# Kernel tuning notes

Measured on AMD Instinct MI355X. Metric: run time of the kernel, lower is better.

The kernel has to match this reference:

```python
import jax, jax.numpy as jnp
import numpy as np

N = 16384      # nodes
E = 524288     # edges (avg degree 32)
F_IN = 128     # input features
H1 = 256       # first_gcn_dimensions
H2 = 256       # second_gcn_dimensions
D1 = 64        # first_dense_neurons
D2 = 2         # second_dense_neurons (fixed by EYE=ones(2))


def setup_inputs() -> dict:
    key = jax.random.key(0)
    ks = jax.random.split(key, 8)
    w = lambda k, shp: (jax.random.normal(k, shp, jnp.float32) * 0.05)
    return dict(
        features=jax.random.normal(ks[0], (N, F_IN), jnp.float32),
        edges=jax.random.randint(ks[1], (2, E), 0, N),
        W1=w(ks[2], (F_IN, H1)), b1=jnp.zeros((H1,), jnp.float32),
        W2=w(ks[3], (H1, H2)), b2=jnp.zeros((H2,), jnp.float32),
        fc1_w=w(ks[4], (D1, H2)), fc1_b=jnp.zeros((D1,), jnp.float32),
        fc2_w=w(ks[5], (D2, D1)), fc2_b=jnp.zeros((D2,), jnp.float32),
    )


def gcn_conv(x, W, b, src, dst, n):
    """PyG GCNConv: xW, add self-loops, symmetric D^-1/2 (A+I) D^-1/2 aggregation."""
    x = x @ W
    loops = jnp.arange(n)
    s = jnp.concatenate([src, loops])
    d = jnp.concatenate([dst, loops])
    deg = jax.ops.segment_sum(jnp.ones(s.shape, x.dtype), d, num_segments=n)
    dinv = jnp.where(deg > 0, jax.lax.rsqrt(deg), 0.0)
    msg = x[s] * (dinv[s] * dinv[d])[:, None]          # gather + scale
    return jax.ops.segment_sum(msg, d, num_segments=n) + b  # scatter-add


def reference(features, edges, W1, b1, W2, b2, fc1_w, fc1_b, fc2_w, fc2_b):
    n = features.shape[0]
    src, dst = edges[0], edges[1]
    h1 = jax.nn.relu(gcn_conv(features, W1, b1, src, dst, n))
    h2 = gcn_conv(h1, W2, b2, src, dst, n)                 # [N, H2]
    a1 = jnp.tanh(h2 @ fc1_w.T + fc1_b)                    # [N, D1]
    assignment = jax.nn.softmax(a1 @ fc2_w.T + fc2_b, axis=1)  # [N, 2]
    group_features = assignment.T @ h2                     # [2, H2]
    # to_dense_adj: dense NxN adjacency, duplicate edges accumulate
    adj = jnp.zeros((n, n), h2.dtype).at[src, dst].add(1.0)
    new_adj = assignment.T @ (adj @ assignment)            # [2, 2]
    positive = jnp.clip(group_features[0][None, :], -100.0, 100.0)
    negative = jnp.clip(group_features[1][None, :], -100.0, 100.0)
    # F.normalize(p=1, dim=1) with eps=1e-12
    denom = jnp.maximum(jnp.sum(jnp.abs(new_adj), axis=1, keepdims=True), 1e-12)
    norm_diag = jnp.diag(new_adj / denom)
    pos_penalty = jnp.mean((norm_diag - 1.0) ** 2)         # MSE vs ones(2)
    graph_embedding = jnp.mean(group_features, axis=0, keepdims=True)  # [1, H2]
    return (graph_embedding, positive, negative, pos_penalty)
```

## Files before the change

### kernel.cpp

```cpp
#include <hip/hip_runtime.h>
#include <hip/hip_bf16.h>
#include <math.h>

#define N_NODES 16384
#define N_EDGES 524288
#define F_IN 128
#define H1 256
#define H2 256
#define D1 64
#define NA_GRID 512
#define DEG_CAP 96
#define SENT 16384

typedef __attribute__((ext_vector_type(8))) short short8;
typedef __attribute__((ext_vector_type(4))) float floatx4;
typedef unsigned short ushort_t;
typedef unsigned int uint_t;

__device__ inline float bf2f(ushort_t u) {
    union { uint_t i; float f; } v;
    v.i = ((uint_t)u) << 16;
    return v.f;
}
__device__ inline float u2f_lo(uint_t u) {
    union { uint_t i; float f; } v;
    v.i = u << 16;
    return v.f;
}
__device__ inline float u2f_hi(uint_t u) {
    union { uint_t i; float f; } v;
    v.i = u & 0xffff0000u;
    return v.f;
}
__device__ inline ushort_t f2bs(float x) {
    __hip_bfloat16 h = __float2bfloat16(x);
    return *reinterpret_cast<ushort_t*>(&h);
}
__device__ inline uint_t pack2(float lo, float hi) {
    return (uint_t)f2bs(lo) | ((uint_t)f2bs(hi) << 16);
}

__global__ __launch_bounds__(256) void prep_fill(
    const int* __restrict__ src, const int* __restrict__ dst,
    const float* __restrict__ W1, const float* __restrict__ W2,
    const float* __restrict__ fc1_w,
    int* __restrict__ cur, ushort_t* __restrict__ col,
    ushort_t* __restrict__ W1t, ushort_t* __restrict__ W2t,
    ushort_t* __restrict__ fc1bf) {
    int b = blockIdx.x, t = threadIdx.x;
    if (b < 2048) {
        int e = b * 256 + t;
        int d = dst[e];
        int pos = atomicAdd(&cur[d], 1);
        if (pos < DEG_CAP) col[d * DEG_CAP + pos] = (ushort_t)src[e];
    } else if (b < 2176) {
        int idx = (b - 2048) * 256 + t;
        int n = idx >> 7, k = idx & 127;
        W1t[idx] = f2bs(W1[k * 256 + n]);
    } else if (b < 2432) {
        int idx = (b - 2176) * 256 + t;
        int n = idx >> 8, k = idx & 255;
        W2t[idx] = f2bs(W2[k * 256 + n]);
    } else {
        int idx = (b - 2432) * 256 + t;
        fc1bf[idx] = f2bs(fc1_w[idx]);
    }
}

__global__ __launch_bounds__(256) void scale_feat(
    const float* __restrict__ features, const int* __restrict__ cnt,
    ushort_t* __restrict__ zs, ushort_t* __restrict__ bufY,
    ushort_t* __restrict__ col) {
    int b = blockIdx.x, t = threadIdx.x;
    if (b == 2048) {
        uint4 z4 = {0u, 0u, 0u, 0u};
        if (t < 16)
            *(uint4*)&zs[(size_t)SENT * 128 + t * 8] = z4;
        else if (t >= 64 && t < 96)
            *(uint4*)&bufY[(size_t)SENT * 256 + (t - 64) * 8] = z4;
        return;
    }
    int gid = b * 256 + t;
    int node = gid >> 5;
    int hl = gid & 31;
    int deg = cnt[node];
    float d = rsqrtf((float)(deg + 1));
    float4 v = *(const float4*)&features[gid * 4];
    uint2 p;
    p.x = pack2(v.x * d, v.y * d);
    p.y = pack2(v.z * d, v.w * d);
    *(uint2*)&zs[gid * 4] = p;
    if (deg < DEG_CAP) {
        int pad = (16 - (deg & 15)) & 15;
        if (hl < pad) col[node * DEG_CAP + deg + hl] = (ushort_t)SENT;
    }
}

__global__ __launch_bounds__(512, 8) void fused_layer1(
    const ushort_t* __restrict__ zs, const int* __restrict__ cnt,
    const ushort_t* __restrict__ col, const float* __restrict__ b1,
    const ushort_t* __restrict__ W1t, const ushort_t* __restrict__ W2t,
    ushort_t* __restrict__ bufY) {
    __shared__ __align__(16) ushort_t Az[16 * 136];
    __shared__ __align__(16) ushort_t Ah[16 * 264];
    const int tid = threadIdx.x;
    const int lane = tid & 63;
    const int wave = tid >> 6;
    const int m = lane & 15;
    const int quad = lane >> 4;
    const int row0 = blockIdx.x * 16;
    const uint_t* colu = (const uint_t*)col;

    for (int ii = 0; ii < 2; ++ii) {
        const int nl = wave * 2 + ii;
        const int node = __builtin_amdgcn_readfirstlane(row0 + nl);
        const int foff = lane * 2;
        const int deg = cnt[node];
        const int nb = (min(deg, DEG_CAP) + 15) >> 4;
        uint_t self = *(const uint_t*)&zs[(size_t)node * 128 + foff];
        float a0 = u2f_lo(self), a1 = u2f_hi(self);
        const int cb = node * (DEG_CAP / 2);
        for (int tb = 0; tb < nb; ++tb) {
            uint_t w[8];
            #pragma unroll
            for (int k = 0; k < 8; ++k) w[k] = colu[cb + tb * 8 + k];
            uint_t g[16];
            #pragma unroll
            for (int k = 0; k < 8; ++k) {
                int j0 = w[k] & 0xffff, j1 = w[k] >> 16;
                g[2 * k]     = *(const uint_t*)&zs[(size_t)j0 * 128 + foff];
                g[2 * k + 1] = *(const uint_t*)&zs[(size_t)j1 * 128 + foff];
            }
            #pragma unroll
            for (int q = 0; q < 16; ++q) {
                a0 += u2f_lo(g[q]); a1 += u2f_hi(g[q]);
            }
        }
        float dn = rsqrtf((float)(deg + 1));
        *(uint_t*)&Az[nl * 136 + foff] = pack2(a0 * dn, a1 * dn);
    }
    __syncthreads();

    const int wcol0 = wave * 32;
    floatx4 acc[2];
    const floatx4 zero4 = {0.f, 0.f, 0.f, 0.f};
    acc[0] = zero4; acc[1] = zero4;
    #pragma unroll
    for (int k0 = 0; k0 < 128; k0 += 32) {
        short8 a = *(const short8*)&Az[m * 136 + k0 + quad * 8];
        #pragma unroll
        for (int j = 0; j < 2; ++j) {
            short8 bb = *(const short8*)
                &W1t[(size_t)(wcol0 + j * 16 + m) * 128 + k0 + quad * 8];
            acc[j] = __builtin_amdgcn_mfma_f32_16x16x32_bf16(a, bb, acc[j], 0, 0, 0);
        }
    }
    #pragma unroll
    for (int j = 0; j < 2; ++j) {
        int cg = wcol0 + j * 16 + m;
        float bv = b1[cg];
        #pragma unroll
        for (int r = 0; r < 4; ++r) {
            float v = fmaxf(acc[j][r] + bv, 0.0f);
            Ah[(quad * 4 + r) * 264 + cg] = f2bs(v);
        }
    }
    __syncthreads();

    acc[0] = zero4; acc[1] = zero4;
    #pragma unroll
    for (int k0 = 0; k0 < 256; k0 += 32) {
        short8 a = *(const short8*)&Ah[m * 264 + k0 + quad * 8];
        #pragma unroll
        for (int j = 0; j < 2; ++j) {
            short8 bb = *(const short8*)
                &W2t[(size_t)(wcol0 + j * 16 + m) * 256 + k0 + quad * 8];
            acc[j] = __builtin_amdgcn_mfma_f32_16x16x32_bf16(a, bb, acc[j], 0, 0, 0);
        }
    }
    float rs4[4];
    #pragma unroll
    for (int r = 0; r < 4; ++r)
        rs4[r] = rsqrtf((float)(cnt[row0 + quad * 4 + r] + 1));
    #pragma unroll
    for (int j = 0; j < 2; ++j) {
        int cg = wcol0 + j * 16 + m;
        #pragma unroll
        for (int r = 0; r < 4; ++r)
            bufY[(size_t)(row0 + quad * 4 + r) * 256 + cg] = f2bs(acc[j][r] * rs4[r]);
    }
}

__global__ __launch_bounds__(512, 8) void agg2(
    const ushort_t* __restrict__ bufY, const int* __restrict__ cnt,
    const ushort_t* __restrict__ col, const float* __restrict__ b2,
    ushort_t* __restrict__ h2buf, int c0) {
    const int tid = threadIdx.x;
    const int lane = tid & 63;
    const int wave = tid >> 6;
    const int node = __builtin_amdgcn_readfirstlane(blockIdx.x * 8 + wave);
    const int coff = c0 + lane * 2;
    const int deg = cnt[node];
    const int nb = (min(deg, DEG_CAP) + 15) >> 4;
    uint_t self = *(const uint_t*)&bufY[(size_t)node * 256 + coff];
    float a0 = u2f_lo(self), a1 = u2f_hi(self);
    const uint_t* colu = (const uint_t*)col;
    const int cb = node * (DEG_CAP / 2);
    for (int tb = 0; tb < nb; ++tb) {
        uint_t w[8];
        #pragma unroll
        for (int k = 0; k < 8; ++k) w[k] = colu[cb + tb * 8 + k];
        uint_t g[16];
        #pragma unroll
        for (int k = 0; k < 8; ++k) {
            int j0 = w[k] & 0xffff, j1 = w[k] >> 16;
            g[2 * k]     = *(const uint_t*)&bufY[(size_t)j0 * 256 + coff];
            g[2 * k + 1] = *(const uint_t*)&bufY[(size_t)j1 * 256 + coff];
        }
        #pragma unroll
        for (int q = 0; q < 16; ++q) {
            a0 += u2f_lo(g[q]); a1 += u2f_hi(g[q]);
        }
    }
    float di = rsqrtf((float)(deg + 1));
    *(uint_t*)&h2buf[(size_t)node * 256 + coff] =
        pack2(a0 * di + b2[coff], a1 * di + b2[coff + 1]);
}

__global__ __launch_bounds__(512) void fused_assign(
    const ushort_t* __restrict__ h2buf,
    const ushort_t* __restrict__ fc1bf, const float* __restrict__ fc1_b,
    const float* __restrict__ fc2_w, const float* __restrict__ fc2_b,
    float* __restrict__ assign, float* __restrict__ gfr) {
    __shared__ __align__(16) ushort_t Ah[16 * 264];
    __shared__ float sha[16][65];
    __shared__ float sas0[16], sas1[16];
    const int tid = threadIdx.x;
    const int lane = tid & 63;
    const int wave = tid >> 6;
    const int m = lane & 15;
    const int quad = lane >> 4;
    const int row0 = blockIdx.x * 16;

    {
        int r = tid >> 5, c = (tid & 31) * 8;
        *(uint4*)&Ah[r * 264 + c] =
            *(const uint4*)&h2buf[(size_t)(row0 + r) * 256 + c];
    }
    __syncthreads();

    if (wave < 4) {
        floatx4 acc = {0.f, 0.f, 0.f, 0.f};
        #pragma unroll
        for (int k0 = 0; k0 < 256; k0 += 32) {
            short8 a = *(const short8*)&Ah[m * 264 + k0 + quad * 8];
            short8 bb = *(const short8*)
                &fc1bf[(size_t)(wave * 16 + m) * 256 + k0 + quad * 8];
            acc = __builtin_amdgcn_mfma_f32_16x16x32_bf16(a, bb, acc, 0, 0, 0);
        }
        int cg = wave * 16 + m;
        float bv = fc1_b[cg];
        #pragma unroll
        for (int r = 0; r < 4; ++r)
            sha[quad * 4 + r][cg] = tanhf(acc[r] + bv);
    }
    __syncthreads();

    if (tid < 16) {
        float p0 = fc2_b[0], p1 = fc2_b[1];
        #pragma unroll 8
        for (int t = 0; t < 64; ++t) {
            float a = sha[tid][t];
            p0 += a * fc2_w[t];
            p1 += a * fc2_w[64 + t];
        }
        float mx = fmaxf(p0, p1);
        float e0 = expf(p0 - mx), e1 = expf(p1 - mx);
        float inv = 1.0f / (e0 + e1);
        float2 as; as.x = e0 * inv; as.y = e1 * inv;
        *(float2*)&assign[(row0 + tid) * 2] = as;
        sas0[tid] = as.x; sas1[tid] = as.y;
    }
    __syncthreads();

    {
        const int f = tid & 255;
        const int which = tid >> 8;
        const float* sv = which ? sas1 : sas0;
        float acc = 0.f;
        #pragma unroll
        for (int i = 0; i < 16; ++i)
            acc += sv[i] * bf2f(Ah[i * 264 + f]);
        float* gfc = gfr + (blockIdx.x & 3) * 512;
        atomicAdd(&gfc[which * 256 + f], acc);
    }
}

__global__ __launch_bounds__(256) void newadj_fin(
    const int* __restrict__ src, const int* __restrict__ dst,
    const float* __restrict__ assign, float* __restrict__ napart,
    int* __restrict__ cntt, const float* __restrict__ gfr,
    float* __restrict__ out) {
    __shared__ float red[4][4];
    __shared__ int sticket;
    const int tid = threadIdx.x;
    const int b = blockIdx.x;
    const int lane = tid & 63;
    const int wave = tid >> 6;

    float a00 = 0.f, a01 = 0.f, a10 = 0.f, a11 = 0.f;
    for (int e = b * 256 + tid; e < N_EDGES; e += NA_GRID * 256) {
        int s = src[e], d = dst[e];
        float s0 = assign[s * 2], s1 = assign[s * 2 + 1];
        float d0 = assign[d * 2], d1 = assign[d * 2 + 1];
        a00 += s0 * d0; a01 += s0 * d1; a10 += s1 * d0; a11 += s1 * d1;
    }
    #pragma unroll
    for (int off = 32; off; off >>= 1) {
        a00 += __shfl_down(a00, off);
        a01 += __shfl_down(a01, off);
        a10 += __shfl_down(a10, off);
        a11 += __shfl_down(a11, off);
    }
    if (lane == 0) {
        red[wave][0] = a00; red[wave][1] = a01;
        red[wave][2] = a10; red[wave][3] = a11;
    }
    __syncthreads();
    if (tid < 4) {
        float v = red[0][tid] + red[1][tid] + red[2][tid] + red[3][tid];
        __hip_atomic_store(&napart[b * 4 + tid], v, __ATOMIC_RELEASE,
                           __HIP_MEMORY_SCOPE_AGENT);
    }
    __syncthreads();
    if (tid == 0)
        sticket = __hip_atomic_fetch_add(cntt, 1, __ATOMIC_ACQ_REL,
                                         __HIP_MEMORY_SCOPE_AGENT);
    __syncthreads();
    if (sticket != NA_GRID - 1) return;

    float acc = 0.f;
    for (int i = lane; i < NA_GRID; i += 64)
        acc += __hip_atomic_load(&napart[i * 4 + wave], __ATOMIC_RELAXED,
                                 __HIP_MEMORY_SCOPE_AGENT);
    #pragma unroll
    for (int off = 32; off; off >>= 1) acc += __shfl_down(acc, off);
    __shared__ float na[4];
    if (lane == 0) na[wave] = acc;
    __syncthreads();
    float g0 = gfr[tid] + gfr[512 + tid] + gfr[1024 + tid] + gfr[1536 + tid];
    float g1 = gfr[256 + tid] + gfr[768 + tid] + gfr[1280 + tid] + gfr[1792 + tid];
    out[tid] = 0.5f * (g0 + g1);
    out[256 + tid] = fminf(fmaxf(g0, -100.f), 100.f);
    out[512 + tid] = fminf(fmaxf(g1, -100.f), 100.f);
    if (tid == 0) {
        float n00 = na[0], n01 = na[1], n10 = na[2], n11 = na[3];
        float den0 = fmaxf(fabsf(n00) + fabsf(n01), 1e-12f);
        float den1 = fmaxf(fabsf(n10) + fabsf(n11), 1e-12f);
        float x0 = n00 / den0 - 1.0f;
        float x1 = n11 / den1 - 1.0f;
        out[768] = 0.5f * (x0 * x0 + x1 * x1);
    }
}


extern "C" void kernel_launch(void* const* d_in, const int* in_sizes, int n_in,
                              void* d_out, int out_size, void* d_ws, size_t ws_size,
                              hipStream_t stream) {
    const float* features = (const float*)d_in[0];
    const int* edges = (const int*)d_in[1];
    const int* src = edges;
    const int* dst = edges + N_EDGES;
    const float* W1 = (const float*)d_in[2];
    const float* b1 = (const float*)d_in[3];
    const float* W2 = (const float*)d_in[4];
    const float* b2 = (const float*)d_in[5];
    const float* fc1_w = (const float*)d_in[6];
    const float* fc1_b = (const float*)d_in[7];
    const float* fc2_w = (const float*)d_in[8];
    const float* fc2_b = (const float*)d_in[9];
    float* out = (float*)d_out;

    char* ws = (char*)d_ws;
    auto carve = [&](size_t bytes) {
        void* q = (void*)ws;
        ws += (bytes + 255) & ~(size_t)255;
        return q;
    };
    int* cur = (int*)carve(N_NODES * 4);
    float* gfr = (float*)carve(4 * 512 * 4);
    int* cnt_na = (int*)carve(256);
    ushort_t* col = (ushort_t*)carve((size_t)N_NODES * DEG_CAP * 2);
    float* assign = (float*)carve(N_NODES * 2 * 4);
    float* napart = (float*)carve(NA_GRID * 4 * 4);
    ushort_t* fc1bf = (ushort_t*)carve(64 * 256 * 2);
    ushort_t* zs = (ushort_t*)carve((size_t)(N_NODES + 1) * F_IN * 2);
    ushort_t* W1t = (ushort_t*)carve(256 * 128 * 2);
    ushort_t* W2t = (ushort_t*)carve(256 * 256 * 2);
    ushort_t* bufY = (ushort_t*)carve((size_t)(N_NODES + 1) * 256 * 2);
    ushort_t* h2buf = (ushort_t*)carve((size_t)N_NODES * 256 * 2);

    hipMemsetAsync(cur, 0, N_NODES * 4 + 4 * 512 * 4 + 256, stream);

    prep_fill<<<2496, 256, 0, stream>>>(src, dst, W1, W2, fc1_w,
                                        cur, col, W1t, W2t, fc1bf);
    scale_feat<<<2049, 256, 0, stream>>>(features, cur, zs, bufY, col);
    fused_layer1<<<N_NODES / 16, 512, 0, stream>>>(
        zs, cur, col, b1, W1t, W2t, bufY);
    agg2<<<N_NODES / 8, 512, 0, stream>>>(bufY, cur, col, b2, h2buf, 0);
    agg2<<<N_NODES / 8, 512, 0, stream>>>(bufY, cur, col, b2, h2buf, 128);
    fused_assign<<<N_NODES / 16, 512, 0, stream>>>(
        h2buf, fc1bf, fc1_b, fc2_w, fc2_b, assign, gfr);
    newadj_fin<<<NA_GRID, 256, 0, stream>>>(src, dst, assign, napart,
                                            cnt_na, gfr, out);
}
```

Before: 196.7 us.

## Fuse layer-2 aggregation into assignment kernel and simplify new_adj reduction

Removes the two agg2 launches and the h2buf round trip by doing the layer-2 gather-aggregation inside fused_assign, with two nodes per wave and 4 features per lane. Neighbor indices are staged in shared memory, and node pairs are interleaved in fused_layer1 too, to overlap gather latency. Since the two softmax outputs sum to one, only p0 is stored and new_adj is rebuilt from three sums (Σs, Σd, Σsd) with one edge-chunk per thread. This adds register pressure, so launch bounds drop to 4 waves per SIMD, and the float subtraction for n11 may cost some precision.

```diff
diff --git a/kernel.cpp b/kernel.cpp
--- a/kernel.cpp
+++ b/kernel.cpp
@@ -96,13 +96,14 @@
     }
 }
 
-__global__ __launch_bounds__(512, 8) void fused_layer1(
+__global__ __launch_bounds__(512, 4) void fused_layer1(
     const ushort_t* __restrict__ zs, const int* __restrict__ cnt,
     const ushort_t* __restrict__ col, const float* __restrict__ b1,
     const ushort_t* __restrict__ W1t, const ushort_t* __restrict__ W2t,
     ushort_t* __restrict__ bufY) {
     __shared__ __align__(16) ushort_t Az[16 * 136];
     __shared__ __align__(16) ushort_t Ah[16 * 264];
+    __shared__ __align__(8) uint_t scol[768];
     const int tid = threadIdx.x;
     const int lane = tid & 63;
     const int wave = tid >> 6;
@@ -111,33 +112,67 @@
     const int row0 = blockIdx.x * 16;
     const uint_t* colu = (const uint_t*)col;
 
-    for (int ii = 0; ii < 2; ++ii) {
-        const int nl = wave * 2 + ii;
-        const int node = __builtin_amdgcn_readfirstlane(row0 + nl);
+    if (tid < 384)
+        *(uint2*)&scol[tid * 2] = *(const uint2*)&colu[row0 * 48 + tid * 2];
+    __syncthreads();
+
+    {
+        const int nl0 = wave * 2, nl1 = wave * 2 + 1;
+        const int node0 = row0 + nl0, node1 = row0 + nl1;
         const int foff = lane * 2;
-        const int deg = cnt[node];
-        const int nb = (min(deg, DEG_CAP) + 15) >> 4;
-        uint_t self = *(const uint_t*)&zs[(size_t)node * 128 + foff];
-        float a0 = u2f_lo(self), a1 = u2f_hi(self);
-        const int cb = node * (DEG_CAP / 2);
-        for (int tb = 0; tb < nb; ++tb) {
-            uint_t w[8];
-            #pragma unroll
-            for (int k = 0; k < 8; ++k) w[k] = colu[cb + tb * 8 + k];
-            uint_t g[16];
-            #pragma unroll
-            for (int k = 0; k < 8; ++k) {
-                int j0 = w[k] & 0xffff, j1 = w[k] >> 16;
-                g[2 * k]     = *(const uint_t*)&zs[(size_t)j0 * 128 + foff];
-                g[2 * k + 1] = *(const uint_t*)&zs[(size_t)j1 * 128 + foff];
-            }
-            #pragma unroll
-            for (int q = 0; q < 16; ++q) {
-                a0 += u2f_lo(g[q]); a1 += u2f_hi(g[q]);
-            }
-        }
-        float dn = rsqrtf((float)(deg + 1));
-        *(uint_t*)&Az[nl * 136 + foff] = pack2(a0 * dn, a1 * dn);
+        const int deg0 = cnt[node0], deg1 = cnt[node1];
+        const int nb0 = (min(deg0, DEG_CAP) + 15) >> 4;
+        const int nb1 = (min(deg1, DEG_CAP) + 15) >> 4;
+        const int nbm = max(nb0, nb1);
+        uint_t s0 = *(const uint_t*)&zs[(size_t)node0 * 128 + foff];
+        uint_t s1 = *(const uint_t*)&zs[(size_t)node1 * 128 + foff];
+        float a00 = u2f_lo(s0), a01 = u2f_hi(s0);
+        float a10 = u2f_lo(s1), a11 = u2f_hi(s1);
+        for (int tb = 0; tb < nbm; ++tb) {
+            const bool p0 = tb < nb0, p1 = tb < nb1;
+            uint_t w0[8], w1[8];
+            if (p0) {
+                #pragma unroll
+                for (int k = 0; k < 8; ++k) w0[k] = scol[nl0 * 48 + tb * 8 + k];
+            }
+            if (p1) {
+                #pragma unroll
+                for (int k = 0; k < 8; ++k) w1[k] = scol[nl1 * 48 + tb * 8 + k];
+            }
+            uint_t g0[16], g1[16];
+            if (p0) {
+                #pragma unroll
+                for (int k = 0; k < 8; ++k) {
+                    int j0 = w0[k] & 0xffff, j1 = w0[k] >> 16;
+                    g0[2 * k]     = *(const uint_t*)&zs[(size_t)j0 * 128 + foff];
+                    g0[2 * k + 1] = *(const uint_t*)&zs[(size_t)j1 * 128 + foff];
+                }
+            }
+            if (p1) {
+                #pragma unroll
+                for (int k = 0; k < 8; ++k) {
+                    int j0 = w1[k] & 0xffff, j1 = w1[k] >> 16;
+                    g1[2 * k]     = *(const uint_t*)&zs[(size_t)j0 * 128 + foff];
+                    g1[2 * k + 1] = *(const uint_t*)&zs[(size_t)j1 * 128 + foff];
+                }
+            }
+            if (p0) {
+                #pragma unroll
+                for (int q = 0; q < 16; ++q) {
+                    a00 += u2f_lo(g0[q]); a01 += u2f_hi(g0[q]);
+                }
+            }
+            if (p1) {
+                #pragma unroll
+                for (int q = 0; q < 16; ++q) {
+                    a10 += u2f_lo(g1[q]); a11 += u2f_hi(g1[q]);
+                }
+            }
+        }
+        float dn0 = rsqrtf((float)(deg0 + 1));
+        float dn1 = rsqrtf((float)(deg1 + 1));
+        *(uint_t*)&Az[nl0 * 136 + foff] = pack2(a00 * dn0, a01 * dn0);
+        *(uint_t*)&Az[nl1 * 136 + foff] = pack2(a10 * dn1, a11 * dn1);
     }
     __syncthreads();
 
@@ -191,48 +226,14 @@
     }
 }
 
-__global__ __launch_bounds__(512, 8) void agg2(
+__global__ __launch_bounds__(512, 4) void fused_assign(
     const ushort_t* __restrict__ bufY, const int* __restrict__ cnt,
     const ushort_t* __restrict__ col, const float* __restrict__ b2,
-    ushort_t* __restrict__ h2buf, int c0) {
-    const int tid = threadIdx.x;
-    const int lane = tid & 63;
-    const int wave = tid >> 6;
-    const int node = __builtin_amdgcn_readfirstlane(blockIdx.x * 8 + wave);
-    const int coff = c0 + lane * 2;
-    const int deg = cnt[node];
-    const int nb = (min(deg, DEG_CAP) + 15) >> 4;
-    uint_t self = *(const uint_t*)&bufY[(size_t)node * 256 + coff];
-    float a0 = u2f_lo(self), a1 = u2f_hi(self);
-    const uint_t* colu = (const uint_t*)col;
-    const int cb = node * (DEG_CAP / 2);
-    for (int tb = 0; tb < nb; ++tb) {
-        uint_t w[8];
-        #pragma unroll
-        for (int k = 0; k < 8; ++k) w[k] = colu[cb + tb * 8 + k];
-        uint_t g[16];
-        #pragma unroll
-        for (int k = 0; k < 8; ++k) {
-            int j0 = w[k] & 0xffff, j1 = w[k] >> 16;
-            g[2 * k]     = *(const uint_t*)&bufY[(size_t)j0 * 256 + coff];
-            g[2 * k + 1] = *(const uint_t*)&bufY[(size_t)j1 * 256 + coff];
-        }
-        #pragma unroll
-        for (int q = 0; q < 16; ++q) {
-            a0 += u2f_lo(g[q]); a1 += u2f_hi(g[q]);
-        }
-    }
-    float di = rsqrtf((float)(deg + 1));
-    *(uint_t*)&h2buf[(size_t)node * 256 + coff] =
-        pack2(a0 * di + b2[coff], a1 * di + b2[coff + 1]);
-}
-
-__global__ __launch_bounds__(512) void fused_assign(
-    const ushort_t* __restrict__ h2buf,
     const ushort_t* __restrict__ fc1bf, const float* __restrict__ fc1_b,
     const float* __restrict__ fc2_w, const float* __restrict__ fc2_b,
-    float* __restrict__ assign, float* __restrict__ gfr) {
+    float* __restrict__ assignp, float* __restrict__ gfr) {
     __shared__ __align__(16) ushort_t Ah[16 * 264];
+    __shared__ __align__(8) uint_t scol[768];
     __shared__ float sha[16][65];
     __shared__ float sas0[16], sas1[16];
     const int tid = threadIdx.x;
@@ -241,11 +242,79 @@
     const int m = lane & 15;
     const int quad = lane >> 4;
     const int row0 = blockIdx.x * 16;
+    const uint_t* colu = (const uint_t*)col;
+
+    if (tid < 384)
+        *(uint2*)&scol[tid * 2] = *(const uint2*)&colu[row0 * 48 + tid * 2];
+    __syncthreads();
 
     {
-        int r = tid >> 5, c = (tid & 31) * 8;
-        *(uint4*)&Ah[r * 264 + c] =
-            *(const uint4*)&h2buf[(size_t)(row0 + r) * 256 + c];
+        const int nl0 = wave * 2, nl1 = wave * 2 + 1;
+        const int node0 = row0 + nl0, node1 = row0 + nl1;
+        const int foff = lane * 4;
+        const int deg0 = cnt[node0], deg1 = cnt[node1];
+        const int nb0 = (min(deg0, DEG_CAP) + 15) >> 4;
+        const int nb1 = (min(deg1, DEG_CAP) + 15) >> 4;
+        const int nbm = max(nb0, nb1);
+        uint2 sv0 = *(const uint2*)&bufY[(size_t)node0 * 256 + foff];
+        uint2 sv1 = *(const uint2*)&bufY[(size_t)node1 * 256 + foff];
+        float a00 = u2f_lo(sv0.x), a01 = u2f_hi(sv0.x);
+        float a02 = u2f_lo(sv0.y), a03 = u2f_hi(sv0.y);
+        float a10 = u2f_lo(sv1.x), a11 = u2f_hi(sv1.x);
+        float a12 = u2f_lo(sv1.y), a13 = u2f_hi(sv1.y);
+        for (int tb = 0; tb < nbm; ++tb) {
+            const bool p0 = tb < nb0, p1 = tb < nb1;
+            uint_t w0[8], w1[8];
+            if (p0) {
+                #pragma unroll
+                for (int k = 0; k < 8; ++k) w0[k] = scol[nl0 * 48 + tb * 8 + k];
+            }
+            if (p1) {
+                #pragma unroll
+                for (int k = 0; k < 8; ++k) w1[k] = scol[nl1 * 48 + tb * 8 + k];
+            }
+            uint2 g0[16], g1[16];
+            if (p0) {
+                #pragma unroll
+                for (int k = 0; k < 8; ++k) {
+                    int j0 = w0[k] & 0xffff, j1 = w0[k] >> 16;
+                    g0[2 * k]     = *(const uint2*)&bufY[(size_t)j0 * 256 + foff];
+                    g0[2 * k + 1] = *(const uint2*)&bufY[(size_t)j1 * 256 + foff];
+                }
+            }
+            if (p1) {
+                #pragma unroll
+                for (int k = 0; k < 8; ++k) {
+                    int j0 = w1[k] & 0xffff, j1 = w1[k] >> 16;
+                    g1[2 * k]     = *(const uint2*)&bufY[(size_t)j0 * 256 + foff];
+                    g1[2 * k + 1] = *(const uint2*)&bufY[(size_t)j1 * 256 + foff];
+                }
+            }
+            if (p0) {
+                #pragma unroll
+                for (int q = 0; q < 16; ++q) {
+                    a00 += u2f_lo(g0[q].x); a01 += u2f_hi(g0[q].x);
+                    a02 += u2f_lo(g0[q].y); a03 += u2f_hi(g0[q].y);
+                }
+            }
+            if (p1) {
+                #pragma unroll
+                for (int q = 0; q < 16; ++q) {
+                    a10 += u2f_lo(g1[q].x); a11 += u2f_hi(g1[q].x);
+                    a12 += u2f_lo(g1[q].y); a13 += u2f_hi(g1[q].y);
+                }
+            }
+        }
+        float di0 = rsqrtf((float)(deg0 + 1));
+        float di1 = rsqrtf((float)(deg1 + 1));
+        float4 bv = *(const float4*)&b2[foff];
+        uint2 pk;
+        pk.x = pack2(a00 * di0 + bv.x, a01 * di0 + bv.y);
+        pk.y = pack2(a02 * di0 + bv.z, a03 * di0 + bv.w);
+        *(uint2*)&Ah[nl0 * 264 + foff] = pk;
+        pk.x = pack2(a10 * di1 + bv.x, a11 * di1 + bv.y);
+        pk.y = pack2(a12 * di1 + bv.z, a13 * di1 + bv.w);
+        *(uint2*)&Ah[nl1 * 264 + foff] = pk;
     }
     __syncthreads();
 
@@ -277,9 +346,8 @@
         float mx = fmaxf(p0, p1);
         float e0 = expf(p0 - mx), e1 = expf(p1 - mx);
         float inv = 1.0f / (e0 + e1);
-        float2 as; as.x = e0 * inv; as.y = e1 * inv;
-        *(float2*)&assign[(row0 + tid) * 2] = as;
-        sas0[tid] = as.x; sas1[tid] = as.y;
+        assignp[row0 + tid] = e0 * inv;
+        sas0[tid] = e0 * inv; sas1[tid] = e1 * inv;
     }
     __syncthreads();
 
@@ -298,36 +366,40 @@
 
 __global__ __launch_bounds__(256) void newadj_fin(
     const int* __restrict__ src, const int* __restrict__ dst,
-    const float* __restrict__ assign, float* __restrict__ napart,
+    const float* __restrict__ assignp, float* __restrict__ napart,
     int* __restrict__ cntt, const float* __restrict__ gfr,
     float* __restrict__ out) {
-    __shared__ float red[4][4];
+    __shared__ float red[4][3];
     __shared__ int sticket;
     const int tid = threadIdx.x;
     const int b = blockIdx.x;
     const int lane = tid & 63;
     const int wave = tid >> 6;
 
-    float a00 = 0.f, a01 = 0.f, a10 = 0.f, a11 = 0.f;
-    for (int e = b * 256 + tid; e < N_EDGES; e += NA_GRID * 256) {
-        int s = src[e], d = dst[e];
-        float s0 = assign[s * 2], s1 = assign[s * 2 + 1];
-        float d0 = assign[d * 2], d1 = assign[d * 2 + 1];
-        a00 += s0 * d0; a01 += s0 * d1; a10 += s1 * d0; a11 += s1 * d1;
+    float ss = 0.f, sd = 0.f, ssd = 0.f;
+    {
+        int g = (b * 256 + tid) * 4;
+        int4 sv = *(const int4*)&src[g];
+        int4 dv = *(const int4*)&dst[g];
+        float s0 = assignp[sv.x], s1 = assignp[sv.y];
+        float s2 = assignp[sv.z], s3 = assignp[sv.w];
+        float d0 = assignp[dv.x], d1 = assignp[dv.y];
+        float d2 = assignp[dv.z], d3 = assignp[dv.w];
+        ss = s0 + s1 + s2 + s3;
+        sd = d0 + d1 + d2 + d3;
+        ssd = s0 * d0 + s1 * d1 + s2 * d2 + s3 * d3;
     }
     #pragma unroll
     for (int off = 32; off; off >>= 1) {
-        a00 += __shfl_down(a00, off);
-        a01 += __shfl_down(a01, off);
-        a10 += __shfl_down(a10, off);
-        a11 += __shfl_down(a11, off);
+        ss += __shfl_down(ss, off);
+        sd += __shfl_down(sd, off);
+        ssd += __shfl_down(ssd, off);
     }
     if (lane == 0) {
-        red[wave][0] = a00; red[wave][1] = a01;
-        red[wave][2] = a10; red[wave][3] = a11;
-    }
-    __syncthreads();
-    if (tid < 4) {
+        red[wave][0] = ssd; red[wave][1] = ss; red[wave][2] = sd;
+    }
+    __syncthreads();
+    if (tid < 3) {
         float v = red[0][tid] + red[1][tid] + red[2][tid] + red[3][tid];
         __hip_atomic_store(&napart[b * 4 + tid], v, __ATOMIC_RELEASE,
                            __HIP_MEMORY_SCOPE_AGENT);
@@ -340,13 +412,15 @@
     if (sticket != NA_GRID - 1) return;
 
     float acc = 0.f;
-    for (int i = lane; i < NA_GRID; i += 64)
-        acc += __hip_atomic_load(&napart[i * 4 + wave], __ATOMIC_RELAXED,
-                                 __HIP_MEMORY_SCOPE_AGENT);
+    if (wave < 3) {
+        for (int i = lane; i < NA_GRID; i += 64)
+            acc += __hip_atomic_load(&napart[i * 4 + wave], __ATOMIC_RELAXED,
+                                     __HIP_MEMORY_SCOPE_AGENT);
+    }
     #pragma unroll
     for (int off = 32; off; off >>= 1) acc += __shfl_down(acc, off);
-    __shared__ float na[4];
-    if (lane == 0) na[wave] = acc;
+    __shared__ float na[3];
+    if (lane == 0 && wave < 3) na[wave] = acc;
     __syncthreads();
     float g0 = gfr[tid] + gfr[512 + tid] + gfr[1024 + tid] + gfr[1536 + tid];
     float g1 = gfr[256 + tid] + gfr[768 + tid] + gfr[1280 + tid] + gfr[1792 + tid];
@@ -354,7 +428,11 @@
     out[256 + tid] = fminf(fmaxf(g0, -100.f), 100.f);
     out[512 + tid] = fminf(fmaxf(g1, -100.f), 100.f);
     if (tid == 0) {
-        float n00 = na[0], n01 = na[1], n10 = na[2], n11 = na[3];
+        float Ssd = na[0], Ss = na[1], Sd = na[2];
+        float n00 = Ssd;
+        float n01 = Ss - Ssd;
+        float n10 = Sd - Ssd;
+        float n11 = (float)N_EDGES - Ss - Sd + Ssd;
         float den0 = fmaxf(fabsf(n00) + fabsf(n01), 1e-12f);
         float den1 = fmaxf(fabsf(n10) + fabsf(n11), 1e-12f);
         float x0 = n00 / den0 - 1.0f;
@@ -391,14 +469,13 @@
     float* gfr = (float*)carve(4 * 512 * 4);
     int* cnt_na = (int*)carve(256);
     ushort_t* col = (ushort_t*)carve((size_t)N_NODES * DEG_CAP * 2);
-    float* assign = (float*)carve(N_NODES * 2 * 4);
+    float* assignp = (float*)carve(N_NODES * 4);
     float* napart = (float*)carve(NA_GRID * 4 * 4);
     ushort_t* fc1bf = (ushort_t*)carve(64 * 256 * 2);
     ushort_t* zs = (ushort_t*)carve((size_t)(N_NODES + 1) * F_IN * 2);
     ushort_t* W1t = (ushort_t*)carve(256 * 128 * 2);
     ushort_t* W2t = (ushort_t*)carve(256 * 256 * 2);
     ushort_t* bufY = (ushort_t*)carve((size_t)(N_NODES + 1) * 256 * 2);
-    ushort_t* h2buf = (ushort_t*)carve((size_t)N_NODES * 256 * 2);
 
     hipMemsetAsync(cur, 0, N_NODES * 4 + 4 * 512 * 4 + 256, stream);
 
@@ -407,10 +484,8 @@
     scale_feat<<<2049, 256, 0, stream>>>(features, cur, zs, bufY, col);
     fused_layer1<<<N_NODES / 16, 512, 0, stream>>>(
         zs, cur, col, b1, W1t, W2t, bufY);
-    agg2<<<N_NODES / 8, 512, 0, stream>>>(bufY, cur, col, b2, h2buf, 0);
-    agg2<<<N_NODES / 8, 512, 0, stream>>>(bufY, cur, col, b2, h2buf, 128);
     fused_assign<<<N_NODES / 16, 512, 0, stream>>>(
-        h2buf, fc1bf, fc1_b, fc2_w, fc2_b, assign, gfr);
-    newadj_fin<<<NA_GRID, 256, 0, stream>>>(src, dst, assign, napart,
+        bufY, cur, col, b2, fc1bf, fc1_b, fc2_w, fc2_b, assignp, gfr);
+    newadj_fin<<<NA_GRID, 256, 0, stream>>>(src, dst, assignp, napart,
                                             cnt_na, gfr, out);
 }
```

Result: no change. 194.0 us (-1.4%).
